# Optimization experiments

Hardware: AMD Instinct MI355X
Metric: run time of the kernel (lower is better)

The kernel has to match this reference:

```python
import jax, jax.numpy as jnp
import numpy as np

B, N, D, H = 2, 2048, 1024, 16
HD = D // H
SCALE = HD ** -0.5


def setup_inputs() -> dict:
    key = jax.random.key(0)
    ks = jax.random.split(key, 9)
    s = D ** -0.5
    return {
        "x": jax.random.normal(ks[0], (B, N, D), dtype=jnp.float32),
        "Wq": jax.random.normal(ks[1], (D, D), dtype=jnp.float32) * s,
        "bq": jax.random.normal(ks[2], (D,), dtype=jnp.float32) * 0.01,
        "Wk": jax.random.normal(ks[3], (D, D), dtype=jnp.float32) * s,
        "bk": jax.random.normal(ks[4], (D,), dtype=jnp.float32) * 0.01,
        "Wv": jax.random.normal(ks[5], (D, D), dtype=jnp.float32) * s,
        "bv": jax.random.normal(ks[6], (D,), dtype=jnp.float32) * 0.01,
        "Wo": jax.random.normal(ks[7], (D, D), dtype=jnp.float32) * s,
        "bo": jax.random.normal(ks[8], (D,), dtype=jnp.float32) * 0.01,
    }


def reference(x, Wq, bq, Wk, bk, Wv, bv, Wo, bo):
    # Q/K/V projections (torch Linear: x @ W.T + b), split into heads: (B,H,N,HD)
    def proj(W, b):
        return (x @ W.T + b).reshape(B, N, H, HD).transpose(0, 2, 1, 3)

    q = proj(Wq, bq)
    k = proj(Wk, bk)
    v = proj(Wv, bv)
    # Scaled dot-product attention with explicit (B,H,N,N) scores
    scores = jnp.einsum("bhnd,bhmd->bhnm", q, k) * SCALE
    attn = jax.nn.softmax(scores, axis=-1)
    y = jnp.einsum("bhnm,bhmd->bhnd", attn, v)
    y = y.transpose(0, 2, 1, 3).reshape(B, N, D)
    # Output projection
    return y @ Wo.T + bo
```

## Files before the change

### kernel.cpp

```cpp
#include <hip/hip_runtime.h>

#define BB 2
#define NN 2048
#define DD 1024
#define HH 16
#define HD 64
#define SCALE 0.125f

typedef unsigned short u16;
typedef unsigned int u32;
typedef __attribute__((ext_vector_type(8))) short short8;
typedef __attribute__((ext_vector_type(4))) float float4v;

__device__ __forceinline__ float b2f(u16 u) {
    union { float f; u32 i; } x; x.i = ((u32)u) << 16; return x.f;
}
__device__ __forceinline__ u16 f2b(float f) {
    union { float f; u32 i; } x; x.f = f;
    u32 i = x.i;
    return (u16)((i + 0x7fffu + ((i >> 16) & 1u)) >> 16);
}

#if __has_builtin(__builtin_amdgcn_exp2f)
#define EXP2F(x) __builtin_amdgcn_exp2f(x)
#else
#define EXP2F(x) __expf((x) * 0.69314718055994531f)
#endif

#if __has_builtin(__builtin_amdgcn_rcpf)
#define RCPF(x) __builtin_amdgcn_rcpf(x)
#else
#define RCPF(x) (1.0f / (x))
#endif

__device__ __forceinline__ void gl_lds16(const u16* g, u16* l) {
    __builtin_amdgcn_global_load_lds(
        (__attribute__((address_space(1))) void*)(void*)g,
        (__attribute__((address_space(3))) void*)l, 16, 0, 0);
}

__global__ __launch_bounds__(256) void cvt_all(
    const float* __restrict__ x,
    const float* __restrict__ Wq, const float* __restrict__ Wk,
    const float* __restrict__ Wv, const float* __restrict__ Wo,
    u16* __restrict__ xb, u16* __restrict__ W4)
{
    int e = (blockIdx.x * 256 + threadIdx.x) * 8;
    const float* s;
    u16* d;
    if (e < 4194304) { s = x + e; d = xb + e; }
    else {
        int e2 = e - 4194304;
        int which = e2 >> 20;
        int off = e2 & 1048575;
        s = ((which == 0) ? Wq : (which == 1) ? Wk : (which == 2) ? Wv : Wo) + off;
        d = W4 + e2;
    }
    float4v a = *(const float4v*)s;
    float4v b = *(const float4v*)(s + 4);
    short8 r;
    r[0] = (short)f2b(a[0]); r[1] = (short)f2b(a[1]);
    r[2] = (short)f2b(a[2]); r[3] = (short)f2b(a[3]);
    r[4] = (short)f2b(b[0]); r[5] = (short)f2b(b[1]);
    r[6] = (short)f2b(b[2]); r[7] = (short)f2b(b[3]);
    *(short8*)d = r;
}


__global__ __launch_bounds__(256) void gemm_qkv(
    const u16* __restrict__ xb,
    const u16* __restrict__ Wqb, const float* __restrict__ bq,
    const u16* __restrict__ Wkb, const float* __restrict__ bk,
    const u16* __restrict__ Wvb, const float* __restrict__ bv,
    u16* __restrict__ Qo, u16* __restrict__ Ko, u16* __restrict__ Vt)
{
    const int tm = blockIdx.y;
    const int tn_all = blockIdx.x;
    const int mat = tn_all >> 3;
    const int tn = tn_all & 7;

    const u16* __restrict__ W     = (mat == 0) ? Wqb : (mat == 1) ? Wkb : Wvb;
    const float* __restrict__ bias = (mat == 0) ? bq : (mat == 1) ? bk : bv;

    __shared__ u16 As[128 * 32];
    __shared__ u16 Bs[128 * 32];

    const int tid  = threadIdx.x;
    const int wave = tid >> 6, lane = tid & 63;
    const int wm = wave >> 1, wn = wave & 1;
    const int quad = lane >> 4, l16 = lane & 15;

    const int r0 = tid >> 2, c0 = tid & 3;
    const int r1 = r0 + 64;

    const u16* ga0 = &xb[(size_t)(tm * 128 + r0) * DD + c0 * 8];
    const u16* ga1 = &xb[(size_t)(tm * 128 + r1) * DD + c0 * 8];
    const u16* gb0 = &W [(size_t)(tn * 128 + r0) * DD + c0 * 8];
    const u16* gb1 = &W [(size_t)(tn * 128 + r1) * DD + c0 * 8];

    float4v acc[4][4] = {};

    for (int k0 = 0; k0 < DD; k0 += 32) {
        __syncthreads();
        gl_lds16(ga0 + k0, &As[tid * 8]);
        gl_lds16(ga1 + k0, &As[(256 + tid) * 8]);
        gl_lds16(gb0 + k0, &Bs[tid * 8]);
        gl_lds16(gb1 + k0, &Bs[(256 + tid) * 8]);
        asm volatile("s_waitcnt vmcnt(0)" ::: "memory");
        __syncthreads();

        short8 af[4], bf[4];
        #pragma unroll
        for (int mi = 0; mi < 4; ++mi)
            af[mi] = *(const short8*)&As[(wm * 64 + mi * 16 + l16) * 32 + quad * 8];
        #pragma unroll
        for (int ni = 0; ni < 4; ++ni)
            bf[ni] = *(const short8*)&Bs[(wn * 64 + ni * 16 + l16) * 32 + quad * 8];

        #pragma unroll
        for (int mi = 0; mi < 4; ++mi)
            #pragma unroll
            for (int ni = 0; ni < 4; ++ni)
                acc[mi][ni] = __builtin_amdgcn_mfma_f32_16x16x32_bf16(
                    af[mi], bf[ni], acc[mi][ni], 0, 0, 0);
    }

    #pragma unroll
    for (int mi = 0; mi < 4; ++mi) {
        #pragma unroll
        for (int ni = 0; ni < 4; ++ni) {
            int cc = tn * 128 + wn * 64 + ni * 16 + l16;
            int h = cc >> 6, hd = cc & 63;
            float bv_ = bias[cc];
            #pragma unroll
            for (int rr = 0; rr < 4; ++rr) {
                int R = tm * 128 + wm * 64 + mi * 16 + quad * 4 + rr;
                int b = R >> 11, n = R & 2047;
                u16 val = f2b(acc[mi][ni][rr] + bv_);
                if (mat == 2) {
                    Vt[(((size_t)(b * HH + h)) * HD + hd) * NN + n] = val;
                } else {
                    u16* Out = (mat == 0) ? Qo : Ko;
                    Out[(((size_t)(b * HH + h)) * NN + n) * HD + hd] = val;
                }
            }
        }
    }
}

__global__ __launch_bounds__(256) void gemm_out(
    const u16* __restrict__ A, const u16* __restrict__ W,
    const float* __restrict__ bias, float* __restrict__ Out)
{
    const int tm = blockIdx.y;
    const int tn = blockIdx.x;

    __shared__ u16 As[2][64 * 32];
    __shared__ u16 Bs[2][128 * 32];

    const int tid  = threadIdx.x;
    const int wave = tid >> 6, lane = tid & 63;
    const int quad = lane >> 4, l16 = lane & 15;
    const int wn = wave;

    const int r0 = tid >> 2, c0 = tid & 3;

    const u16* ga  = &A[(size_t)(tm * 64 + r0) * DD + c0 * 8];
    const u16* gb0 = &W[(size_t)(tn * 128 + r0) * DD + c0 * 8];
    const u16* gb1 = &W[(size_t)(tn * 128 + r0 + 64) * DD + c0 * 8];

    float4v acc[4][2] = {};

    gl_lds16(ga,  &As[0][tid * 8]);
    gl_lds16(gb0, &Bs[0][tid * 8]);
    gl_lds16(gb1, &Bs[0][(256 + tid) * 8]);

    int cur = 0;
    for (int k0 = 0; k0 < DD; k0 += 32) {
        __syncthreads();
        const int kn = (k0 + 32) & (DD - 1);
        gl_lds16(ga + kn,  &As[cur ^ 1][tid * 8]);
        gl_lds16(gb0 + kn, &Bs[cur ^ 1][tid * 8]);
        gl_lds16(gb1 + kn, &Bs[cur ^ 1][(256 + tid) * 8]);

        short8 af[4], bf[2];
        #pragma unroll
        for (int mi = 0; mi < 4; ++mi)
            af[mi] = *(const short8*)&As[cur][(mi * 16 + l16) * 32 + quad * 8];
        #pragma unroll
        for (int ni = 0; ni < 2; ++ni)
            bf[ni] = *(const short8*)&Bs[cur][(wn * 32 + ni * 16 + l16) * 32 + quad * 8];

        #pragma unroll
        for (int mi = 0; mi < 4; ++mi)
            #pragma unroll
            for (int ni = 0; ni < 2; ++ni)
                acc[mi][ni] = __builtin_amdgcn_mfma_f32_16x16x32_bf16(
                    af[mi], bf[ni], acc[mi][ni], 0, 0, 0);
        cur ^= 1;
    }
    asm volatile("s_waitcnt vmcnt(0)" ::: "memory");

    #pragma unroll
    for (int mi = 0; mi < 4; ++mi) {
        #pragma unroll
        for (int ni = 0; ni < 2; ++ni) {
            int cc = tn * 128 + wn * 32 + ni * 16 + l16;
            float bv_ = bias[cc];
            #pragma unroll
            for (int rr = 0; rr < 4; ++rr) {
                int R = tm * 64 + mi * 16 + quad * 4 + rr;
                Out[(size_t)R * DD + cc] = acc[mi][ni][rr] + bv_;
            }
        }
    }
}

__global__ __launch_bounds__(256, 4) void attn_mfma(
    const u16* __restrict__ Q, const u16* __restrict__ K,
    const u16* __restrict__ Vt, u16* __restrict__ Y)
{
    const int id   = blockIdx.x;
    const int xcd  = id & 7;
    const int slot = id >> 3;
    const int bh   = (xcd << 2) | (slot & 3);
    const int qb   = slot >> 2;

    const int tid = threadIdx.x;
    const int wave = tid >> 6, lane = tid & 63;
    const int quad = lane >> 4, l16 = lane & 15;

    const u16* __restrict__ Qb = Q + (size_t)bh * NN * HD;
    const u16* __restrict__ Kb = K + (size_t)bh * NN * HD;
    const u16* __restrict__ Vb = Vt + (size_t)bh * HD * NN;

    __shared__ u16 Ks[2][64 * 64];
    __shared__ u16 Vs[64 * 64];
    __shared__ u16 Ps[4][16 * 72];

    short8 qa[2];
    {
        int qrow = qb * 64 + wave * 16 + l16;
        #pragma unroll
        for (int kc = 0; kc < 2; ++kc) {
            short8 t = *(const short8*)&Qb[(size_t)qrow * HD + kc * 32 + quad * 8];
            #pragma unroll
            for (int j = 0; j < 8; ++j)
                qa[kc][j] = (short)f2b(b2f((u16)t[j]) * SCALE);
        }
    }

    short8 onesB;
    #pragma unroll
    for (int j = 0; j < 8; ++j) onesB[j] = (short)0x3F80;

    float4v oc[4] = {};
    float4v la = {};

    const int srow = tid >> 3, sslot = tid & 7;
    const int oA = (sslot + srow) & 7;
    const int oB = (sslot + srow + 32) & 7;

    const int fs0 = ((quad - l16) & 7) * 8;
    const int fs1 = ((4 + quad - l16) & 7) * 8;

    gl_lds16(&Kb[(size_t)srow * HD + oA * 8],        &Ks[0][tid * 8]);
    gl_lds16(&Kb[(size_t)(srow + 32) * HD + oB * 8], &Ks[0][(256 + tid) * 8]);

    for (int k0 = 0; k0 < NN; k0 += 64) {
        const int cur = (k0 >> 6) & 1;
        const int kn = (k0 + 64) & (NN - 1);

        __syncthreads();

        gl_lds16(&Vb[(size_t)srow * NN + k0 + oA * 8],        &Vs[tid * 8]);
        gl_lds16(&Vb[(size_t)(srow + 32) * NN + k0 + oB * 8], &Vs[(256 + tid) * 8]);
        gl_lds16(&Kb[(size_t)(kn + srow) * HD + oA * 8],      &Ks[cur ^ 1][tid * 8]);
        gl_lds16(&Kb[(size_t)(kn + srow + 32) * HD + oB * 8], &Ks[cur ^ 1][(256 + tid) * 8]);

        float4v sc[4];
        #pragma unroll
        for (int kt = 0; kt < 4; ++kt) {
            short8 kb0 = *(const short8*)&Ks[cur][(kt * 16 + l16) * 64 + fs0];
            short8 kb1 = *(const short8*)&Ks[cur][(kt * 16 + l16) * 64 + fs1];
            float4v z = {};
            z = __builtin_amdgcn_mfma_f32_16x16x32_bf16(qa[0], kb0, z, 0, 0, 0);
            sc[kt] = __builtin_amdgcn_mfma_f32_16x16x32_bf16(qa[1], kb1, z, 0, 0, 0);
        }

        #pragma unroll
        for (int rr = 0; rr < 4; ++rr) {
            #pragma unroll
            for (int kt = 0; kt < 4; ++kt) {
                float p = EXP2F(__builtin_fmaf(sc[kt][rr], 1.44269504f,
                                               -11.5415603f));
                union { float f; u32 i; } px; px.f = p;
                Ps[wave][(quad * 4 + rr) * 72 + kt * 16 + l16] = (u16)(px.i >> 16);
            }
        }
        asm volatile("s_waitcnt lgkmcnt(0)" ::: "memory");

        short8 pa0 = *(const short8*)&Ps[wave][l16 * 72 + quad * 8];
        short8 pa1 = *(const short8*)&Ps[wave][l16 * 72 + 32 + quad * 8];

        la = __builtin_amdgcn_mfma_f32_16x16x32_bf16(pa0, onesB, la, 0, 0, 0);
        la = __builtin_amdgcn_mfma_f32_16x16x32_bf16(pa1, onesB, la, 0, 0, 0);

        __syncthreads();

        #pragma unroll
        for (int ht = 0; ht < 4; ++ht) {
            short8 vb0 = *(const short8*)&Vs[(ht * 16 + l16) * 64 + fs0];
            short8 vb1 = *(const short8*)&Vs[(ht * 16 + l16) * 64 + fs1];
            oc[ht] = __builtin_amdgcn_mfma_f32_16x16x32_bf16(pa0, vb0, oc[ht], 0, 0, 0);
            oc[ht] = __builtin_amdgcn_mfma_f32_16x16x32_bf16(pa1, vb1, oc[ht], 0, 0, 0);
        }
    }

    const int b = bh >> 4, h = bh & 15;
    float inv[4];
    #pragma unroll
    for (int rr = 0; rr < 4; ++rr) inv[rr] = RCPF(la[rr]);
    #pragma unroll
    for (int ht = 0; ht < 4; ++ht) {
        #pragma unroll
        for (int rr = 0; rr < 4; ++rr) {
            int n = qb * 64 + wave * 16 + quad * 4 + rr;
            int col = h * HD + ht * 16 + l16;
            Y[((size_t)(b * NN + n)) * DD + col] = f2b(oc[ht][rr] * inv[rr]);
        }
    }
}

extern "C" void kernel_launch(void* const* d_in, const int* in_sizes, int n_in,
                              void* d_out, int out_size, void* d_ws, size_t ws_size,
                              hipStream_t stream) {
    const float* x  = (const float*)d_in[0];
    const float* Wq = (const float*)d_in[1];
    const float* bq = (const float*)d_in[2];
    const float* Wk = (const float*)d_in[3];
    const float* bk = (const float*)d_in[4];
    const float* Wv = (const float*)d_in[5];
    const float* bv = (const float*)d_in[6];
    const float* Wo = (const float*)d_in[7];
    const float* bo = (const float*)d_in[8];
    float* out = (float*)d_out;

    const size_t M1 = 1024 * 1024;
    u16* base = (u16*)d_ws;
    u16* xb  = base;
    u16* W4  = base + 4 * M1;
    u16* Wqb = W4;
    u16* Wkb = W4 + 1 * M1;
    u16* Wvb = W4 + 2 * M1;
    u16* Wob = W4 + 3 * M1;
    u16* Qw  = base + 8 * M1;
    u16* Kw  = base + 12 * M1;
    u16* Vtw = base + 16 * M1;
    u16* Yw  = xb;

    cvt_all<<<dim3(4096), 256, 0, stream>>>(x, Wq, Wk, Wv, Wo, xb, W4);

    gemm_qkv<<<dim3(24, 32), 256, 0, stream>>>(xb, Wqb, bq, Wkb, bk, Wvb, bv,
                                               Qw, Kw, Vtw);

    attn_mfma<<<dim3(1024), 256, 0, stream>>>(Qw, Kw, Vtw, Yw);

    gemm_out<<<dim3(8, 64), 256, 0, stream>>>(Yw, Wob, bo, out);
}
```

Measured before the change: 210.8 us.

## Use 32x32 MFMA in attention with register P, double-buffer V and QKV GEMM tiles

The attention kernel moves to 32x32x16 MFMA tiles with 128 query rows per block. The scores are computed transposed (K times Q), so the exponentiated probabilities can be packed and swapped between lanes with shuffles instead of going through LDS. V is now double-buffered like K, one of the two barriers per step is removed, and the grid is halved. The QKV GEMM also double-buffers its LDS tiles so the next K-slice loads while the current one computes. The trade-offs are higher register pressure, since the occupancy hint of four blocks was dropped, and fewer blocks in the attention grid.

```diff
diff --git a/kernel.cpp b/kernel.cpp
--- a/kernel.cpp
+++ b/kernel.cpp
@@ -11,6 +11,7 @@
 typedef unsigned int u32;
 typedef __attribute__((ext_vector_type(8))) short short8;
 typedef __attribute__((ext_vector_type(4))) float float4v;
+typedef __attribute__((ext_vector_type(16))) float f32x16;
 
 __device__ __forceinline__ float b2f(u16 u) {
     union { float f; u32 i; } x; x.i = ((u32)u) << 16; return x.f;
@@ -82,8 +83,8 @@
     const u16* __restrict__ W     = (mat == 0) ? Wqb : (mat == 1) ? Wkb : Wvb;
     const float* __restrict__ bias = (mat == 0) ? bq : (mat == 1) ? bk : bv;
 
-    __shared__ u16 As[128 * 32];
-    __shared__ u16 Bs[128 * 32];
+    __shared__ u16 As[2][128 * 32];
+    __shared__ u16 Bs[2][128 * 32];
 
     const int tid  = threadIdx.x;
     const int wave = tid >> 6, lane = tid & 63;
@@ -100,22 +101,27 @@
 
     float4v acc[4][4] = {};
 
+    gl_lds16(ga0, &As[0][tid * 8]);
+    gl_lds16(ga1, &As[0][(256 + tid) * 8]);
+    gl_lds16(gb0, &Bs[0][tid * 8]);
+    gl_lds16(gb1, &Bs[0][(256 + tid) * 8]);
+
+    int cur = 0;
     for (int k0 = 0; k0 < DD; k0 += 32) {
         __syncthreads();
-        gl_lds16(ga0 + k0, &As[tid * 8]);
-        gl_lds16(ga1 + k0, &As[(256 + tid) * 8]);
-        gl_lds16(gb0 + k0, &Bs[tid * 8]);
-        gl_lds16(gb1 + k0, &Bs[(256 + tid) * 8]);
-        asm volatile("s_waitcnt vmcnt(0)" ::: "memory");
-        __syncthreads();
+        const int kn = (k0 + 32) & (DD - 1);
+        gl_lds16(ga0 + kn, &As[cur ^ 1][tid * 8]);
+        gl_lds16(ga1 + kn, &As[cur ^ 1][(256 + tid) * 8]);
+        gl_lds16(gb0 + kn, &Bs[cur ^ 1][tid * 8]);
+        gl_lds16(gb1 + kn, &Bs[cur ^ 1][(256 + tid) * 8]);
 
         short8 af[4], bf[4];
         #pragma unroll
         for (int mi = 0; mi < 4; ++mi)
-            af[mi] = *(const short8*)&As[(wm * 64 + mi * 16 + l16) * 32 + quad * 8];
+            af[mi] = *(const short8*)&As[cur][(wm * 64 + mi * 16 + l16) * 32 + quad * 8];
         #pragma unroll
         for (int ni = 0; ni < 4; ++ni)
-            bf[ni] = *(const short8*)&Bs[(wn * 64 + ni * 16 + l16) * 32 + quad * 8];
+            bf[ni] = *(const short8*)&Bs[cur][(wn * 64 + ni * 16 + l16) * 32 + quad * 8];
 
         #pragma unroll
         for (int mi = 0; mi < 4; ++mi)
@@ -123,7 +129,9 @@
             for (int ni = 0; ni < 4; ++ni)
                 acc[mi][ni] = __builtin_amdgcn_mfma_f32_16x16x32_bf16(
                     af[mi], bf[ni], acc[mi][ni], 0, 0, 0);
-    }
+        cur ^= 1;
+    }
+    asm volatile("s_waitcnt vmcnt(0)" ::: "memory");
 
     #pragma unroll
     for (int mi = 0; mi < 4; ++mi) {
@@ -216,7 +224,7 @@
     }
 }
 
-__global__ __launch_bounds__(256, 4) void attn_mfma(
+__global__ __launch_bounds__(256) void attn_mfma(
     const u16* __restrict__ Q, const u16* __restrict__ K,
     const u16* __restrict__ Vt, u16* __restrict__ Y)
 {
@@ -226,27 +234,26 @@
     const int bh   = (xcd << 2) | (slot & 3);
     const int qb   = slot >> 2;
 
-    const int tid = threadIdx.x;
+    const int tid  = threadIdx.x;
     const int wave = tid >> 6, lane = tid & 63;
-    const int quad = lane >> 4, l16 = lane & 15;
+    const int l31  = lane & 31, hi = lane >> 5;
 
     const u16* __restrict__ Qb = Q + (size_t)bh * NN * HD;
     const u16* __restrict__ Kb = K + (size_t)bh * NN * HD;
     const u16* __restrict__ Vb = Vt + (size_t)bh * HD * NN;
 
     __shared__ u16 Ks[2][64 * 64];
-    __shared__ u16 Vs[64 * 64];
-    __shared__ u16 Ps[4][16 * 72];
-
-    short8 qa[2];
+    __shared__ u16 Vs[2][64 * 64];
+
+    short8 qf[4];
     {
-        int qrow = qb * 64 + wave * 16 + l16;
-        #pragma unroll
-        for (int kc = 0; kc < 2; ++kc) {
-            short8 t = *(const short8*)&Qb[(size_t)qrow * HD + kc * 32 + quad * 8];
+        int qrow = qb * 128 + wave * 32 + l31;
+        #pragma unroll
+        for (int c = 0; c < 4; ++c) {
+            short8 t = *(const short8*)&Qb[(size_t)qrow * HD + c * 16 + hi * 8];
             #pragma unroll
             for (int j = 0; j < 8; ++j)
-                qa[kc][j] = (short)f2b(b2f((u16)t[j]) * SCALE);
+                qf[c][j] = (short)f2b(b2f((u16)t[j]) * SCALE);
         }
     }
 
@@ -254,18 +261,17 @@
     #pragma unroll
     for (int j = 0; j < 8; ++j) onesB[j] = (short)0x3F80;
 
-    float4v oc[4] = {};
-    float4v la = {};
+    f32x16 oc[2] = {};
+    f32x16 la = {};
 
     const int srow = tid >> 3, sslot = tid & 7;
     const int oA = (sslot + srow) & 7;
     const int oB = (sslot + srow + 32) & 7;
 
-    const int fs0 = ((quad - l16) & 7) * 8;
-    const int fs1 = ((4 + quad - l16) & 7) * 8;
-
-    gl_lds16(&Kb[(size_t)srow * HD + oA * 8],        &Ks[0][tid * 8]);
-    gl_lds16(&Kb[(size_t)(srow + 32) * HD + oB * 8], &Ks[0][(256 + tid) * 8]);
+    gl_lds16(&Kb[(size_t)srow * HD + oA * 8],          &Ks[0][tid * 8]);
+    gl_lds16(&Kb[(size_t)(srow + 32) * HD + oB * 8],   &Ks[0][(256 + tid) * 8]);
+    gl_lds16(&Vb[(size_t)srow * NN + oA * 8],          &Vs[0][tid * 8]);
+    gl_lds16(&Vb[(size_t)(srow + 32) * NN + oB * 8],   &Vs[0][(256 + tid) * 8]);
 
     for (int k0 = 0; k0 < NN; k0 += 64) {
         const int cur = (k0 >> 6) & 1;
@@ -273,61 +279,91 @@
 
         __syncthreads();
 
-        gl_lds16(&Vb[(size_t)srow * NN + k0 + oA * 8],        &Vs[tid * 8]);
-        gl_lds16(&Vb[(size_t)(srow + 32) * NN + k0 + oB * 8], &Vs[(256 + tid) * 8]);
         gl_lds16(&Kb[(size_t)(kn + srow) * HD + oA * 8],      &Ks[cur ^ 1][tid * 8]);
         gl_lds16(&Kb[(size_t)(kn + srow + 32) * HD + oB * 8], &Ks[cur ^ 1][(256 + tid) * 8]);
-
-        float4v sc[4];
-        #pragma unroll
-        for (int kt = 0; kt < 4; ++kt) {
-            short8 kb0 = *(const short8*)&Ks[cur][(kt * 16 + l16) * 64 + fs0];
-            short8 kb1 = *(const short8*)&Ks[cur][(kt * 16 + l16) * 64 + fs1];
-            float4v z = {};
-            z = __builtin_amdgcn_mfma_f32_16x16x32_bf16(qa[0], kb0, z, 0, 0, 0);
-            sc[kt] = __builtin_amdgcn_mfma_f32_16x16x32_bf16(qa[1], kb1, z, 0, 0, 0);
-        }
-
-        #pragma unroll
-        for (int rr = 0; rr < 4; ++rr) {
-            #pragma unroll
-            for (int kt = 0; kt < 4; ++kt) {
-                float p = EXP2F(__builtin_fmaf(sc[kt][rr], 1.44269504f,
-                                               -11.5415603f));
-                union { float f; u32 i; } px; px.f = p;
-                Ps[wave][(quad * 4 + rr) * 72 + kt * 16 + l16] = (u16)(px.i >> 16);
+        gl_lds16(&Vb[(size_t)srow * NN + kn + oA * 8],        &Vs[cur ^ 1][tid * 8]);
+        gl_lds16(&Vb[(size_t)(srow + 32) * NN + kn + oB * 8], &Vs[cur ^ 1][(256 + tid) * 8]);
+
+        f32x16 st[2];
+        __builtin_amdgcn_s_setprio(1);
+        #pragma unroll
+        for (int kt = 0; kt < 2; ++kt) {
+            f32x16 z = {};
+            const int row = kt * 32 + l31;
+            #pragma unroll
+            for (int c = 0; c < 4; ++c) {
+                short8 kf = *(const short8*)
+                    &Ks[cur][row * 64 + ((2 * c + hi - row) & 7) * 8];
+                z = __builtin_amdgcn_mfma_f32_32x32x16_bf16(kf, qf[c], z, 0, 0, 0);
             }
-        }
-        asm volatile("s_waitcnt lgkmcnt(0)" ::: "memory");
-
-        short8 pa0 = *(const short8*)&Ps[wave][l16 * 72 + quad * 8];
-        short8 pa1 = *(const short8*)&Ps[wave][l16 * 72 + 32 + quad * 8];
-
-        la = __builtin_amdgcn_mfma_f32_16x16x32_bf16(pa0, onesB, la, 0, 0, 0);
-        la = __builtin_amdgcn_mfma_f32_16x16x32_bf16(pa1, onesB, la, 0, 0, 0);
-
-        __syncthreads();
-
-        #pragma unroll
-        for (int ht = 0; ht < 4; ++ht) {
-            short8 vb0 = *(const short8*)&Vs[(ht * 16 + l16) * 64 + fs0];
-            short8 vb1 = *(const short8*)&Vs[(ht * 16 + l16) * 64 + fs1];
-            oc[ht] = __builtin_amdgcn_mfma_f32_16x16x32_bf16(pa0, vb0, oc[ht], 0, 0, 0);
-            oc[ht] = __builtin_amdgcn_mfma_f32_16x16x32_bf16(pa1, vb1, oc[ht], 0, 0, 0);
-        }
-    }
+            st[kt] = z;
+        }
+        __builtin_amdgcn_s_setprio(0);
+
+        u32 pk0[8], pk1[8];
+        #pragma unroll
+        for (int i = 0; i < 8; ++i) {
+            union { float f; u32 i; } a, b;
+            a.f = EXP2F(__builtin_fmaf(st[0][2 * i],     1.44269504f, -11.5415603f));
+            b.f = EXP2F(__builtin_fmaf(st[0][2 * i + 1], 1.44269504f, -11.5415603f));
+            pk0[i] = (a.i >> 16) | (b.i & 0xFFFF0000u);
+            a.f = EXP2F(__builtin_fmaf(st[1][2 * i],     1.44269504f, -11.5415603f));
+            b.f = EXP2F(__builtin_fmaf(st[1][2 * i + 1], 1.44269504f, -11.5415603f));
+            pk1[i] = (a.i >> 16) | (b.i & 0xFFFF0000u);
+        }
+
+        short8 pa[4];
+        #pragma unroll
+        for (int kt = 0; kt < 2; ++kt) {
+            const u32* pk = (kt == 0) ? pk0 : pk1;
+            u32 sA = hi ? pk[0] : pk[2];
+            u32 sB = hi ? pk[1] : pk[3];
+            u32 sC = hi ? pk[4] : pk[6];
+            u32 sD = hi ? pk[5] : pk[7];
+            u32 rA = (u32)__shfl_xor((int)sA, 32, 64);
+            u32 rB = (u32)__shfl_xor((int)sB, 32, 64);
+            u32 rC = (u32)__shfl_xor((int)sC, 32, 64);
+            u32 rD = (u32)__shfl_xor((int)sD, 32, 64);
+            union { u32 w[4]; short8 s; } lo, hi_;
+            lo.w[0] = hi ? rA : pk[0];
+            lo.w[1] = hi ? rB : pk[1];
+            lo.w[2] = hi ? pk[2] : rA;
+            lo.w[3] = hi ? pk[3] : rB;
+            hi_.w[0] = hi ? rC : pk[4];
+            hi_.w[1] = hi ? rD : pk[5];
+            hi_.w[2] = hi ? pk[6] : rC;
+            hi_.w[3] = hi ? pk[7] : rD;
+            pa[2 * kt]     = lo.s;
+            pa[2 * kt + 1] = hi_.s;
+        }
+
+        __builtin_amdgcn_s_setprio(1);
+        #pragma unroll
+        for (int ks = 0; ks < 4; ++ks)
+            la = __builtin_amdgcn_mfma_f32_32x32x16_bf16(pa[ks], onesB, la, 0, 0, 0);
+        #pragma unroll
+        for (int ks = 0; ks < 4; ++ks) {
+            #pragma unroll
+            for (int ht = 0; ht < 2; ++ht) {
+                const int row = ht * 32 + l31;
+                short8 vf = *(const short8*)
+                    &Vs[cur][row * 64 + ((2 * ks + hi - row) & 7) * 8];
+                oc[ht] = __builtin_amdgcn_mfma_f32_32x32x16_bf16(pa[ks], vf, oc[ht], 0, 0, 0);
+            }
+        }
+        __builtin_amdgcn_s_setprio(0);
+    }
+    asm volatile("s_waitcnt vmcnt(0)" ::: "memory");
 
     const int b = bh >> 4, h = bh & 15;
-    float inv[4];
     #pragma unroll
-    for (int rr = 0; rr < 4; ++rr) inv[rr] = RCPF(la[rr]);
-    #pragma unroll
-    for (int ht = 0; ht < 4; ++ht) {
-        #pragma unroll
-        for (int rr = 0; rr < 4; ++rr) {
-            int n = qb * 64 + wave * 16 + quad * 4 + rr;
-            int col = h * HD + ht * 16 + l16;
-            Y[((size_t)(b * NN + n)) * DD + col] = f2b(oc[ht][rr] * inv[rr]);
+    for (int r = 0; r < 16; ++r) {
+        const int n = qb * 128 + wave * 32 + (r & 3) + 8 * (r >> 2) + 4 * hi;
+        const float iv = RCPF(la[r]);
+        #pragma unroll
+        for (int ht = 0; ht < 2; ++ht) {
+            const int col = h * HD + ht * 32 + l31;
+            Y[((size_t)(b * NN + n)) * DD + col] = f2b(oc[ht][r] * iv);
         }
     }
 }
@@ -364,7 +400,7 @@
     gemm_qkv<<<dim3(24, 32), 256, 0, stream>>>(xb, Wqb, bq, Wkb, bk, Wvb, bv,
                                                Qw, Kw, Vtw);
 
-    attn_mfma<<<dim3(1024), 256, 0, stream>>>(Qw, Kw, Vtw, Yw);
+    attn_mfma<<<dim3(512), 256, 0, stream>>>(Qw, Kw, Vtw, Yw);
 
     gemm_out<<<dim3(8, 64), 256, 0, stream>>>(Yw, Wob, bo, out);
 }
```

After: 209.1 us. Within noise of the previous version (-0.8%).

## Double-buffer QKV GEMM and attention V tiles, widen attention blocks to 8 waves

Applied to the files above, without the earlier changes.

The QKV GEMM now prefetches the next K-slice into a second LDS buffer while computing the current one, and writes transposed V with 4-wide vector stores. The attention kernel uses 512-thread blocks covering 128 query rows and double-buffers V alongside K, which removes the mid-loop barrier. It also wraps the MFMA sections in s_setprio to favor matrix issue. The risks are higher LDS use and fewer blocks, which could lower occupancy, and reliance on implicit waits for async LDS loads.

```diff
diff --git a/kernel.cpp b/kernel.cpp
--- a/kernel.cpp
+++ b/kernel.cpp
@@ -9,6 +9,7 @@
 
 typedef unsigned short u16;
 typedef unsigned int u32;
+typedef __attribute__((ext_vector_type(4))) short short4v;
 typedef __attribute__((ext_vector_type(8))) short short8;
 typedef __attribute__((ext_vector_type(4))) float float4v;
 
@@ -82,8 +83,8 @@
     const u16* __restrict__ W     = (mat == 0) ? Wqb : (mat == 1) ? Wkb : Wvb;
     const float* __restrict__ bias = (mat == 0) ? bq : (mat == 1) ? bk : bv;
 
-    __shared__ u16 As[128 * 32];
-    __shared__ u16 Bs[128 * 32];
+    __shared__ u16 As[2][128 * 32];
+    __shared__ u16 Bs[2][128 * 32];
 
     const int tid  = threadIdx.x;
     const int wave = tid >> 6, lane = tid & 63;
@@ -100,22 +101,27 @@
 
     float4v acc[4][4] = {};
 
+    gl_lds16(ga0, &As[0][tid * 8]);
+    gl_lds16(ga1, &As[0][(256 + tid) * 8]);
+    gl_lds16(gb0, &Bs[0][tid * 8]);
+    gl_lds16(gb1, &Bs[0][(256 + tid) * 8]);
+
+    int cur = 0;
     for (int k0 = 0; k0 < DD; k0 += 32) {
         __syncthreads();
-        gl_lds16(ga0 + k0, &As[tid * 8]);
-        gl_lds16(ga1 + k0, &As[(256 + tid) * 8]);
-        gl_lds16(gb0 + k0, &Bs[tid * 8]);
-        gl_lds16(gb1 + k0, &Bs[(256 + tid) * 8]);
-        asm volatile("s_waitcnt vmcnt(0)" ::: "memory");
-        __syncthreads();
+        const int kn = (k0 + 32) & (DD - 1);
+        gl_lds16(ga0 + kn, &As[cur ^ 1][tid * 8]);
+        gl_lds16(ga1 + kn, &As[cur ^ 1][(256 + tid) * 8]);
+        gl_lds16(gb0 + kn, &Bs[cur ^ 1][tid * 8]);
+        gl_lds16(gb1 + kn, &Bs[cur ^ 1][(256 + tid) * 8]);
 
         short8 af[4], bf[4];
         #pragma unroll
         for (int mi = 0; mi < 4; ++mi)
-            af[mi] = *(const short8*)&As[(wm * 64 + mi * 16 + l16) * 32 + quad * 8];
+            af[mi] = *(const short8*)&As[cur][(wm * 64 + mi * 16 + l16) * 32 + quad * 8];
         #pragma unroll
         for (int ni = 0; ni < 4; ++ni)
-            bf[ni] = *(const short8*)&Bs[(wn * 64 + ni * 16 + l16) * 32 + quad * 8];
+            bf[ni] = *(const short8*)&Bs[cur][(wn * 64 + ni * 16 + l16) * 32 + quad * 8];
 
         #pragma unroll
         for (int mi = 0; mi < 4; ++mi)
@@ -123,7 +129,9 @@
             for (int ni = 0; ni < 4; ++ni)
                 acc[mi][ni] = __builtin_amdgcn_mfma_f32_16x16x32_bf16(
                     af[mi], bf[ni], acc[mi][ni], 0, 0, 0);
-    }
+        cur ^= 1;
+    }
+    asm volatile("s_waitcnt vmcnt(0)" ::: "memory");
 
     #pragma unroll
     for (int mi = 0; mi < 4; ++mi) {
@@ -132,16 +140,22 @@
             int cc = tn * 128 + wn * 64 + ni * 16 + l16;
             int h = cc >> 6, hd = cc & 63;
             float bv_ = bias[cc];
-            #pragma unroll
-            for (int rr = 0; rr < 4; ++rr) {
-                int R = tm * 128 + wm * 64 + mi * 16 + quad * 4 + rr;
-                int b = R >> 11, n = R & 2047;
-                u16 val = f2b(acc[mi][ni][rr] + bv_);
-                if (mat == 2) {
-                    Vt[(((size_t)(b * HH + h)) * HD + hd) * NN + n] = val;
-                } else {
-                    u16* Out = (mat == 0) ? Qo : Ko;
-                    Out[(((size_t)(b * HH + h)) * NN + n) * HD + hd] = val;
+            if (mat == 2) {
+                short4v v4;
+                #pragma unroll
+                for (int rr = 0; rr < 4; ++rr)
+                    v4[rr] = (short)f2b(acc[mi][ni][rr] + bv_);
+                int R0 = tm * 128 + wm * 64 + mi * 16 + quad * 4;
+                int b = R0 >> 11, n = R0 & 2047;
+                *(short4v*)&Vt[(((size_t)(b * HH + h)) * HD + hd) * NN + n] = v4;
+            } else {
+                u16* Out = (mat == 0) ? Qo : Ko;
+                #pragma unroll
+                for (int rr = 0; rr < 4; ++rr) {
+                    int R = tm * 128 + wm * 64 + mi * 16 + quad * 4 + rr;
+                    int b = R >> 11, n = R & 2047;
+                    Out[(((size_t)(b * HH + h)) * NN + n) * HD + hd] =
+                        f2b(acc[mi][ni][rr] + bv_);
                 }
             }
         }
@@ -216,7 +230,7 @@
     }
 }
 
-__global__ __launch_bounds__(256, 4) void attn_mfma(
+__global__ __launch_bounds__(512) void attn_mfma(
     const u16* __restrict__ Q, const u16* __restrict__ K,
     const u16* __restrict__ Vt, u16* __restrict__ Y)
 {
@@ -226,7 +240,7 @@
     const int bh   = (xcd << 2) | (slot & 3);
     const int qb   = slot >> 2;
 
-    const int tid = threadIdx.x;
+    const int tid  = threadIdx.x;
     const int wave = tid >> 6, lane = tid & 63;
     const int quad = lane >> 4, l16 = lane & 15;
 
@@ -235,12 +249,12 @@
     const u16* __restrict__ Vb = Vt + (size_t)bh * HD * NN;
 
     __shared__ u16 Ks[2][64 * 64];
-    __shared__ u16 Vs[64 * 64];
-    __shared__ u16 Ps[4][16 * 72];
+    __shared__ u16 Vs[2][64 * 64];
+    __shared__ u16 Ps[8][16 * 72];
 
     short8 qa[2];
     {
-        int qrow = qb * 64 + wave * 16 + l16;
+        int qrow = qb * 128 + wave * 16 + l16;
         #pragma unroll
         for (int kc = 0; kc < 2; ++kc) {
             short8 t = *(const short8*)&Qb[(size_t)qrow * HD + kc * 32 + quad * 8];
@@ -258,14 +272,13 @@
     float4v la = {};
 
     const int srow = tid >> 3, sslot = tid & 7;
-    const int oA = (sslot + srow) & 7;
-    const int oB = (sslot + srow + 32) & 7;
+    const int oct = (sslot + srow) & 7;
 
     const int fs0 = ((quad - l16) & 7) * 8;
     const int fs1 = ((4 + quad - l16) & 7) * 8;
 
-    gl_lds16(&Kb[(size_t)srow * HD + oA * 8],        &Ks[0][tid * 8]);
-    gl_lds16(&Kb[(size_t)(srow + 32) * HD + oB * 8], &Ks[0][(256 + tid) * 8]);
+    gl_lds16(&Kb[(size_t)srow * HD + oct * 8], &Ks[0][tid * 8]);
+    gl_lds16(&Vb[(size_t)srow * NN + oct * 8], &Vs[0][tid * 8]);
 
     for (int k0 = 0; k0 < NN; k0 += 64) {
         const int cur = (k0 >> 6) & 1;
@@ -273,12 +286,11 @@
 
         __syncthreads();
 
-        gl_lds16(&Vb[(size_t)srow * NN + k0 + oA * 8],        &Vs[tid * 8]);
-        gl_lds16(&Vb[(size_t)(srow + 32) * NN + k0 + oB * 8], &Vs[(256 + tid) * 8]);
-        gl_lds16(&Kb[(size_t)(kn + srow) * HD + oA * 8],      &Ks[cur ^ 1][tid * 8]);
-        gl_lds16(&Kb[(size_t)(kn + srow + 32) * HD + oB * 8], &Ks[cur ^ 1][(256 + tid) * 8]);
+        gl_lds16(&Kb[(size_t)(kn + srow) * HD + oct * 8], &Ks[cur ^ 1][tid * 8]);
+        gl_lds16(&Vb[(size_t)srow * NN + kn + oct * 8],   &Vs[cur ^ 1][tid * 8]);
 
         float4v sc[4];
+        __builtin_amdgcn_s_setprio(1);
         #pragma unroll
         for (int kt = 0; kt < 4; ++kt) {
             short8 kb0 = *(const short8*)&Ks[cur][(kt * 16 + l16) * 64 + fs0];
@@ -287,6 +299,7 @@
             z = __builtin_amdgcn_mfma_f32_16x16x32_bf16(qa[0], kb0, z, 0, 0, 0);
             sc[kt] = __builtin_amdgcn_mfma_f32_16x16x32_bf16(qa[1], kb1, z, 0, 0, 0);
         }
+        __builtin_amdgcn_s_setprio(0);
 
         #pragma unroll
         for (int rr = 0; rr < 4; ++rr) {
@@ -303,19 +316,19 @@
         short8 pa0 = *(const short8*)&Ps[wave][l16 * 72 + quad * 8];
         short8 pa1 = *(const short8*)&Ps[wave][l16 * 72 + 32 + quad * 8];
 
+        __builtin_amdgcn_s_setprio(1);
         la = __builtin_amdgcn_mfma_f32_16x16x32_bf16(pa0, onesB, la, 0, 0, 0);
         la = __builtin_amdgcn_mfma_f32_16x16x32_bf16(pa1, onesB, la, 0, 0, 0);
-
-        __syncthreads();
-
         #pragma unroll
         for (int ht = 0; ht < 4; ++ht) {
-            short8 vb0 = *(const short8*)&Vs[(ht * 16 + l16) * 64 + fs0];
-            short8 vb1 = *(const short8*)&Vs[(ht * 16 + l16) * 64 + fs1];
+            short8 vb0 = *(const short8*)&Vs[cur][(ht * 16 + l16) * 64 + fs0];
+            short8 vb1 = *(const short8*)&Vs[cur][(ht * 16 + l16) * 64 + fs1];
             oc[ht] = __builtin_amdgcn_mfma_f32_16x16x32_bf16(pa0, vb0, oc[ht], 0, 0, 0);
             oc[ht] = __builtin_amdgcn_mfma_f32_16x16x32_bf16(pa1, vb1, oc[ht], 0, 0, 0);
         }
-    }
+        __builtin_amdgcn_s_setprio(0);
+    }
+    asm volatile("s_waitcnt vmcnt(0)" ::: "memory");
 
     const int b = bh >> 4, h = bh & 15;
     float inv[4];
@@ -325,7 +338,7 @@
     for (int ht = 0; ht < 4; ++ht) {
         #pragma unroll
         for (int rr = 0; rr < 4; ++rr) {
-            int n = qb * 64 + wave * 16 + quad * 4 + rr;
+            int n = qb * 128 + wave * 16 + quad * 4 + rr;
             int col = h * HD + ht * 16 + l16;
             Y[((size_t)(b * NN + n)) * DD + col] = f2b(oc[ht][rr] * inv[rr]);
         }
@@ -364,7 +377,7 @@
     gemm_qkv<<<dim3(24, 32), 256, 0, stream>>>(xb, Wqb, bq, Wkb, bk, Wvb, bv,
                                                Qw, Kw, Vtw);
 
-    attn_mfma<<<dim3(1024), 256, 0, stream>>>(Qw, Kw, Vtw, Yw);
+    attn_mfma<<<dim3(512), 512, 0, stream>>>(Qw, Kw, Vtw, Yw);
 
     gemm_out<<<dim3(8, 64), 256, 0, stream>>>(Yw, Wob, bo, out);
 }
```

Result: no change. 214.8 us (+1.9%).
